# Optimization experiments

Hardware: AMD Instinct MI355X
Metric: run time of the kernel (lower is better)

The kernel has to match this reference:

```python
import jax, jax.numpy as jnp
import numpy as np

B, T, D, HD = 256, 256, 384, 64  # batch, seq_len, embedding_dim, head_dim


def setup_inputs() -> dict:
    key = jax.random.key(0)
    k1, k2, k3, k4 = jax.random.split(key, 4)
    x = jax.random.normal(k1, (B, T, D), dtype=jnp.float32)
    # nn.Linear(D, HD, bias=False) weight shape is [HD, D]; init scaled like kaiming-uniform magnitude
    Wq = jax.random.normal(k2, (HD, D), dtype=jnp.float32) * (1.0 / np.sqrt(D))
    Wk = jax.random.normal(k3, (HD, D), dtype=jnp.float32) * (1.0 / np.sqrt(D))
    Wv = jax.random.normal(k4, (HD, D), dtype=jnp.float32) * (1.0 / np.sqrt(D))
    return {"x": x, "Wq": Wq, "Wk": Wk, "Wv": Wv}


def reference(x, Wq, Wk, Wv):
    # Projections: x @ W^T  (Linear with bias=False)
    q = jnp.einsum('btd,hd->bth', x, Wq)  # [B,T,HD]
    k = jnp.einsum('btd,hd->bth', x, Wk)
    v = jnp.einsum('btd,hd->bth', x, Wv)
    scale = 1.0 / np.sqrt(HD).astype(np.float32)
    scores = jnp.einsum('bqh,bkh->bqk', q, k) * scale  # [B,T,T]
    T_ = x.shape[1]
    causal = jnp.tril(jnp.ones((T_, T_), dtype=bool))
    scores = jnp.where(causal, scores, jnp.float32(-jnp.inf))
    attn = jax.nn.softmax(scores, axis=-1)
    # dropout disabled (eval mode) for deterministic reference
    return jnp.einsum('bqk,bkh->bqh', attn, v)
```

## Files before the change

kernel.cpp:

```cpp
#include <hip/hip_runtime.h>

typedef __attribute__((ext_vector_type(8))) short bf16x8;
typedef __attribute__((ext_vector_type(4))) float f32x4;

__device__ inline unsigned short f2bf(float f) {
    unsigned u = __float_as_uint(f);
    return (unsigned short)((u + 0x7fffu + ((u >> 16) & 1u)) >> 16);
}
__device__ inline void gload16(const void* g, void* l) {
    __builtin_amdgcn_global_load_lds(
        (const __attribute__((address_space(1))) unsigned*)g,
        (__attribute__((address_space(3))) unsigned*)l, 16, 0, 0);
}

__global__ void wconv(const float* __restrict__ Wq, const float* __restrict__ Wk,
                      const float* __restrict__ Wv, short* __restrict__ Wp) {
    int i = blockIdx.x * 256 + threadIdx.x;
    if (i >= 192 * 384) return;
    int col = i / 384;
    int k   = i - col * 384;
    const float* src = col < 64 ? (Wq + col * 384)
                     : col < 128 ? (Wk + (col - 64) * 384)
                                 : (Wv + (col - 128) * 384);
    int kc = k >> 5, g = (k >> 3) & 3, kl = k & 7;
    Wp[kc * 6144 + (((g * 192 + col) ^ g) << 3) + kl] = (short)f2bf(src[k]);
}

__global__ __launch_bounds__(1024) void fused_attn(
    const float* __restrict__ x, const short* __restrict__ Wp,
    float* __restrict__ out) {
    __shared__ short LDSH[45568];
    short* const Ksh = LDSH;
    short* const Vt  = LDSH + 18432;
    short* const Pb  = LDSH + 35328;
    short* const wst = LDSH;
    short* const xst = LDSH + 18432;

    const int tid = threadIdx.x;
    const int wv = tid >> 6, lane = tid & 63;
    const int g = lane >> 4, c = lane & 15;
    const int b = blockIdx.x;
    const int q0 = wv * 16;

    const int xr0 = tid >> 3;
    const int xc4 = tid & 7;
    const float* gx0 = x + ((size_t)b * 256 + xr0) * 384 + xc4 * 4;
    const float* gx1 = gx0 + (size_t)128 * 384;

    f32x4 acc[12];
#pragma unroll
    for (int j = 0; j < 12; ++j) acc[j] = (f32x4){0.f, 0.f, 0.f, 0.f};

#define STAGE_W(S, BUF)                                                       \
    if (wv < 12) gload16(Wp + (S) * 6144 + wv * 512 + lane * 8,               \
                         wst + (BUF) * 6144 + wv * 512);
#define XWRITE(BUF, A, Bv)                                                    \
    {                                                                         \
        uint2 p0_, p1_;                                                       \
        p0_.x = (unsigned)f2bf((A).x) | ((unsigned)f2bf((A).y) << 16);        \
        p0_.y = (unsigned)f2bf((A).z) | ((unsigned)f2bf((A).w) << 16);        \
        p1_.x = (unsigned)f2bf((Bv).x) | ((unsigned)f2bf((Bv).y) << 16);      \
        p1_.y = (unsigned)f2bf((Bv).z) | ((unsigned)f2bf((Bv).w) << 16);      \
        *(uint2*)&xst[(BUF) * 10240 + xr0 * 40 + xc4 * 4] = p0_;              \
        *(uint2*)&xst[(BUF) * 10240 + (xr0 + 128) * 40 + xc4 * 4] = p1_;      \
    }
#define COMPUTE(S)                                                            \
    {                                                                         \
        const short* xb = xst + ((S) & 1) * 10240;                            \
        const short* wb = wst + ((S) & 1) * 6144;                             \
        bf16x8 af = *(const bf16x8*)&xb[(q0 + c) * 40 + g * 8];               \
        _Pragma("unroll")                                                     \
        for (int h_ = 0; h_ < 2; ++h_) {                                      \
            bf16x8 bfr[6];                                                    \
            _Pragma("unroll")                                                 \
            for (int j6 = 0; j6 < 6; ++j6) {                                  \
                int col = (h_ * 6 + j6) * 16 + c;                             \
                bfr[j6] = *(const bf16x8*)&wb[((g * 192 + col) ^ g) << 3];    \
            }                                                                 \
            _Pragma("unroll")                                                 \
            for (int j6 = 0; j6 < 6; ++j6)                                    \
                acc[h_ * 6 + j6] = __builtin_amdgcn_mfma_f32_16x16x32_bf16(   \
                    af, bfr[j6], acc[h_ * 6 + j6], 0, 0, 0);                  \
    }                                                                         \
    }
#define STEP(S, LX0, LX1, WX0, WX1)                                          \
    {                                                                        \
        STAGE_W((S) + 1, ((S) + 1) & 1)                                      \
        __builtin_amdgcn_sched_barrier(0);                                   \
        if ((S) <= 9) {                                                      \
            LX0 = *(const float4*)(gx0 + ((S) + 2) * 32);                    \
            LX1 = *(const float4*)(gx1 + ((S) + 2) * 32);                    \
        }                                                                    \
        __builtin_amdgcn_sched_barrier(0);                                   \
        COMPUTE(S)                                                           \
        XWRITE(((S) + 1) & 1, WX0, WX1)                                      \
        if (wv < 12) {                                                       \
            if ((S) <= 9) asm volatile("s_waitcnt vmcnt(2)" ::: "memory");   \
            else          asm volatile("s_waitcnt vmcnt(0)" ::: "memory");   \
        }                                                                    \
        asm volatile("s_waitcnt lgkmcnt(0)" ::: "memory");                   \
        __builtin_amdgcn_s_barrier();                                        \
        __builtin_amdgcn_sched_barrier(0);                                   \
    }

    float4 xA0, xA1, xB0, xB1, xC0, xC1;

    xA0 = *(const float4*)(gx0);
    xA1 = *(const float4*)(gx1);
    __builtin_amdgcn_sched_barrier(0);
    STAGE_W(0, 0)
    __builtin_amdgcn_sched_barrier(0);
    xB0 = *(const float4*)(gx0 + 32);
    xB1 = *(const float4*)(gx1 + 32);
    __builtin_amdgcn_sched_barrier(0);
    XWRITE(0, xA0, xA1)
    if (wv < 12) asm volatile("s_waitcnt vmcnt(2)" ::: "memory");
    asm volatile("s_waitcnt lgkmcnt(0)" ::: "memory");
    __builtin_amdgcn_s_barrier();
    __builtin_amdgcn_sched_barrier(0);

    STEP(0, xC0, xC1, xB0, xB1)
    STEP(1, xA0, xA1, xC0, xC1)
    STEP(2, xB0, xB1, xA0, xA1)
    STEP(3, xC0, xC1, xB0, xB1)
    STEP(4, xA0, xA1, xC0, xC1)
    STEP(5, xB0, xB1, xA0, xA1)
    STEP(6, xC0, xC1, xB0, xB1)
    STEP(7, xA0, xA1, xC0, xC1)
    STEP(8, xB0, xB1, xA0, xA1)
    STEP(9, xC0, xC1, xB0, xB1)
    STEP(10, xA0, xA1, xC0, xC1)
    COMPUTE(11)
    __syncthreads();

    short* const pbw = Pb + wv * 640;
    bf16x8 qf0, qf1;
    {
#pragma unroll
        for (int r = 0; r < 4; ++r) {
            pbw[(4 * g + r) * 40 + c]      = (short)f2bf(acc[0][r]);
            pbw[(4 * g + r) * 40 + 16 + c] = (short)f2bf(acc[1][r]);
        }
        qf0 = *(const bf16x8*)&pbw[c * 40 + g * 8];
#pragma unroll
        for (int r = 0; r < 4; ++r) {
            pbw[(4 * g + r) * 40 + c]      = (short)f2bf(acc[2][r]);
            pbw[(4 * g + r) * 40 + 16 + c] = (short)f2bf(acc[3][r]);
        }
        qf1 = *(const bf16x8*)&pbw[c * 40 + g * 8];
    }
#pragma unroll
    for (int nj = 4; nj < 8; ++nj) {
        const int row = q0 + 4 * g;
#pragma unroll
        for (int r = 0; r < 4; ++r)
            Ksh[(row + r) * 72 + (nj - 4) * 16 + c] = (short)f2bf(acc[nj][r]);
    }
#pragma unroll
    for (int nj = 8; nj < 12; ++nj) {
        const int h = (nj - 8) * 16 + c;
        const int swz = ((h >> 3) & 7) << 3;
        const int row = q0 + 4 * g;
#pragma unroll
        for (int r = 0; r < 4; ++r)
            Vt[(h * 264 + row + r) ^ swz] = (short)f2bf(acc[nj][r]);
    }
    __syncthreads();

    {
        f32x4 o[4];
#pragma unroll
        for (int nj = 0; nj < 4; ++nj) o[nj] = (f32x4){0.f, 0.f, 0.f, 0.f};
        float m[4] = {-INFINITY, -INFINITY, -INFINITY, -INFINITY};
        float ls[4] = {0.f, 0.f, 0.f, 0.f};
        const int jmax = (q0 + 15) >> 5;

        for (int j = 0; j <= jmax; ++j) {
            f32x4 s0 = {0.f, 0.f, 0.f, 0.f}, s1 = {0.f, 0.f, 0.f, 0.f};
            {
                bf16x8 kf;
                kf = *(const bf16x8*)&Ksh[(32 * j + c) * 72 + g * 8];
                s0 = __builtin_amdgcn_mfma_f32_16x16x32_bf16(qf0, kf, s0, 0, 0, 0);
                kf = *(const bf16x8*)&Ksh[(32 * j + c) * 72 + 32 + g * 8];
                s0 = __builtin_amdgcn_mfma_f32_16x16x32_bf16(qf1, kf, s0, 0, 0, 0);
                kf = *(const bf16x8*)&Ksh[(32 * j + 16 + c) * 72 + g * 8];
                s1 = __builtin_amdgcn_mfma_f32_16x16x32_bf16(qf0, kf, s1, 0, 0, 0);
                kf = *(const bf16x8*)&Ksh[(32 * j + 16 + c) * 72 + 32 + g * 8];
                s1 = __builtin_amdgcn_mfma_f32_16x16x32_bf16(qf1, kf, s1, 0, 0, 0);
            }
            float t0[4], t1[4];
#pragma unroll
            for (int r = 0; r < 4; ++r) {
                t0[r] = s0[r] * 0.125f;
                t1[r] = s1[r] * 0.125f;
            }
            if (j == jmax) {
                int q = q0 + 4 * g;
#pragma unroll
                for (int r = 0; r < 4; ++r) {
                    if (32 * j + c > q + r) t0[r] = -INFINITY;
                    if (32 * j + 16 + c > q + r) t1[r] = -INFINITY;
                }
            }
            float corr[4], p0[4], p1[4];
#pragma unroll
            for (int r = 0; r < 4; ++r) {
                float v = fmaxf(t0[r], t1[r]);
#pragma unroll
                for (int off = 1; off < 16; off <<= 1) v = fmaxf(v, __shfl_xor(v, off, 16));
                float mn = fmaxf(m[r], v);
                corr[r] = __expf(m[r] - mn);
                m[r] = mn;
                p0[r] = __expf(t0[r] - mn);
                p1[r] = __expf(t1[r] - mn);
                float rs = p0[r] + p1[r];
#pragma unroll
                for (int off = 1; off < 16; off <<= 1) rs += __shfl_xor(rs, off, 16);
                ls[r] = ls[r] * corr[r] + rs;
            }
#pragma unroll
            for (int nj = 0; nj < 4; ++nj) {
                f32x4 t = o[nj];
                t[0] *= corr[0]; t[1] *= corr[1]; t[2] *= corr[2]; t[3] *= corr[3];
                o[nj] = t;
            }
#pragma unroll
            for (int r = 0; r < 4; ++r) {
                pbw[(4 * g + r) * 40 + c]      = (short)f2bf(p0[r]);
                pbw[(4 * g + r) * 40 + 16 + c] = (short)f2bf(p1[r]);
            }
            bf16x8 pfa = *(const bf16x8*)&pbw[c * 40 + g * 8];
#pragma unroll
            for (int nj = 0; nj < 4; ++nj) {
                int h = 16 * nj + c;
                int swz = ((2 * nj + (c >> 3)) & 7) << 3;
                bf16x8 vf = *(const bf16x8*)&Vt[(h * 264 + 32 * j + g * 8) ^ swz];
                o[nj] = __builtin_amdgcn_mfma_f32_16x16x32_bf16(pfa, vf, o[nj], 0, 0, 0);
            }
        }
        float inv[4];
#pragma unroll
        for (int r = 0; r < 4; ++r) inv[r] = 1.f / ls[r];
        float* ob = out + ((size_t)b * 256 + q0) * 64;
#pragma unroll
        for (int nj = 0; nj < 4; ++nj)
#pragma unroll
            for (int r = 0; r < 4; ++r)
                ob[(4 * g + r) * 64 + 16 * nj + c] = o[nj][r] * inv[r];
    }
#undef STAGE_W
#undef XWRITE
#undef COMPUTE
#undef STEP
}

extern "C" void kernel_launch(void* const* d_in, const int* in_sizes, int n_in,
                              void* d_out, int out_size, void* d_ws, size_t ws_size,
                              hipStream_t stream) {
    const float* x  = (const float*)d_in[0];
    const float* Wq = (const float*)d_in[1];
    const float* Wk = (const float*)d_in[2];
    const float* Wv = (const float*)d_in[3];
    float* out = (float*)d_out;

    short* Wp = (short*)d_ws;

    wconv<<<dim3(288), dim3(256), 0, stream>>>(Wq, Wk, Wv, Wp);
    fused_attn<<<dim3(256), dim3(1024), 0, stream>>>(x, Wp, out);
}
```

Measured before the change: 41.10 us.

## Retile projection GEMM to 64x48 per-wave blocks and stage Q through LDS

The QKV projection GEMM tiling changes from each wave owning 16 rows by all 192 columns to a 4x4 wave grid in which each wave owns a 64x48 output tile. Per K step each wave now reads 4 A fragments and 3 B fragments for 12 MFMAs instead of 1 A and 12 B, which cuts LDS read traffic. Because a wave no longer holds its own Q rows, Q is written to a new LDS region and read back before attention. This raises shared memory use from about 89KB to 125KB and adds a Q store-and-reload round trip.

```diff
diff --git a/kernel.cpp b/kernel.cpp
--- a/kernel.cpp
+++ b/kernel.cpp
@@ -29,27 +29,32 @@
 __global__ __launch_bounds__(1024) void fused_attn(
     const float* __restrict__ x, const short* __restrict__ Wp,
     float* __restrict__ out) {
-    __shared__ short LDSH[45568];
-    short* const Ksh = LDSH;
-    short* const Vt  = LDSH + 18432;
-    short* const Pb  = LDSH + 35328;
-    short* const wst = LDSH;
-    short* const xst = LDSH + 18432;
+    __shared__ short LDSH[64000];
+    short* const Qlds = LDSH;
+    short* const Ksh  = LDSH + 18432;
+    short* const Vt   = LDSH + 36864;
+    short* const Pb   = LDSH + 53760;
+    short* const wst  = LDSH;
+    short* const xst  = LDSH + 18432;
 
     const int tid = threadIdx.x;
     const int wv = tid >> 6, lane = tid & 63;
     const int g = lane >> 4, c = lane & 15;
     const int b = blockIdx.x;
     const int q0 = wv * 16;
+    const int wm2 = (wv >> 2) * 64;
+    const int wn2 = (wv & 3) * 48;
 
     const int xr0 = tid >> 3;
     const int xc4 = tid & 7;
     const float* gx0 = x + ((size_t)b * 256 + xr0) * 384 + xc4 * 4;
     const float* gx1 = gx0 + (size_t)128 * 384;
 
-    f32x4 acc[12];
-#pragma unroll
-    for (int j = 0; j < 12; ++j) acc[j] = (f32x4){0.f, 0.f, 0.f, 0.f};
+    f32x4 acc[4][3];
+#pragma unroll
+    for (int i = 0; i < 4; ++i)
+#pragma unroll
+        for (int j = 0; j < 3; ++j) acc[i][j] = (f32x4){0.f, 0.f, 0.f, 0.f};
 
 #define STAGE_W(S, BUF)                                                       \
     if (wv < 12) gload16(Wp + (S) * 6144 + wv * 512 + lane * 8,               \
@@ -68,28 +73,29 @@
     {                                                                         \
         const short* xb = xst + ((S) & 1) * 10240;                            \
         const short* wb = wst + ((S) & 1) * 6144;                             \
-        bf16x8 af = *(const bf16x8*)&xb[(q0 + c) * 40 + g * 8];               \
+        bf16x8 af[4], bfr[3];                                                 \
         _Pragma("unroll")                                                     \
-        for (int h_ = 0; h_ < 2; ++h_) {                                      \
-            bf16x8 bfr[6];                                                    \
+        for (int mi = 0; mi < 4; ++mi)                                        \
+            af[mi] = *(const bf16x8*)&xb[(wm2 + 16 * mi + c) * 40 + g * 8];   \
+        _Pragma("unroll")                                                     \
+        for (int nj = 0; nj < 3; ++nj) {                                      \
+            int col = wn2 + nj * 16 + c;                                      \
+            bfr[nj] = *(const bf16x8*)&wb[((g * 192 + col) ^ g) << 3];        \
+        }                                                                     \
+        _Pragma("unroll")                                                     \
+        for (int mi = 0; mi < 4; ++mi)                                        \
             _Pragma("unroll")                                                 \
-            for (int j6 = 0; j6 < 6; ++j6) {                                  \
-                int col = (h_ * 6 + j6) * 16 + c;                             \
-                bfr[j6] = *(const bf16x8*)&wb[((g * 192 + col) ^ g) << 3];    \
-            }                                                                 \
-            _Pragma("unroll")                                                 \
-            for (int j6 = 0; j6 < 6; ++j6)                                    \
-                acc[h_ * 6 + j6] = __builtin_amdgcn_mfma_f32_16x16x32_bf16(   \
-                    af, bfr[j6], acc[h_ * 6 + j6], 0, 0, 0);                  \
-    }                                                                         \
-    }
-#define STEP(S, LX0, LX1, WX0, WX1)                                          \
+            for (int nj = 0; nj < 3; ++nj)                                    \
+                acc[mi][nj] = __builtin_amdgcn_mfma_f32_16x16x32_bf16(        \
+                    af[mi], bfr[nj], acc[mi][nj], 0, 0, 0);                   \
+    }
+#define STEP(S, LD0, LD1, WX0, WX1)                                          \
     {                                                                        \
         STAGE_W((S) + 1, ((S) + 1) & 1)                                      \
         __builtin_amdgcn_sched_barrier(0);                                   \
         if ((S) <= 9) {                                                      \
-            LX0 = *(const float4*)(gx0 + ((S) + 2) * 32);                    \
-            LX1 = *(const float4*)(gx1 + ((S) + 2) * 32);                    \
+            LD0 = *(const float4*)(gx0 + ((S) + 2) * 32);                    \
+            LD1 = *(const float4*)(gx1 + ((S) + 2) * 32);                    \
         }                                                                    \
         __builtin_amdgcn_sched_barrier(0);                                   \
         COMPUTE(S)                                                           \
@@ -133,41 +139,35 @@
     COMPUTE(11)
     __syncthreads();
 
-    short* const pbw = Pb + wv * 640;
-    bf16x8 qf0, qf1;
+#pragma unroll
+    for (int mi = 0; mi < 4; ++mi) {
+#pragma unroll
+        for (int nj = 0; nj < 3; ++nj) {
+            const int colb = wn2 + nj * 16;
+            const int row = wm2 + 16 * mi + 4 * g;
+            if (colb < 64) {
+#pragma unroll
+                for (int r = 0; r < 4; ++r)
+                    Qlds[(row + r) * 72 + colb + c] = (short)f2bf(acc[mi][nj][r]);
+            } else if (colb < 128) {
+#pragma unroll
+                for (int r = 0; r < 4; ++r)
+                    Ksh[(row + r) * 72 + (colb - 64) + c] = (short)f2bf(acc[mi][nj][r]);
+            } else {
+                const int h = colb - 128 + c;
+                const int swz = ((h >> 3) & 7) << 3;
+#pragma unroll
+                for (int r = 0; r < 4; ++r)
+                    Vt[(h * 264 + row + r) ^ swz] = (short)f2bf(acc[mi][nj][r]);
+            }
+        }
+    }
+    __syncthreads();
+
     {
-#pragma unroll
-        for (int r = 0; r < 4; ++r) {
-            pbw[(4 * g + r) * 40 + c]      = (short)f2bf(acc[0][r]);
-            pbw[(4 * g + r) * 40 + 16 + c] = (short)f2bf(acc[1][r]);
-        }
-        qf0 = *(const bf16x8*)&pbw[c * 40 + g * 8];
-#pragma unroll
-        for (int r = 0; r < 4; ++r) {
-            pbw[(4 * g + r) * 40 + c]      = (short)f2bf(acc[2][r]);
-            pbw[(4 * g + r) * 40 + 16 + c] = (short)f2bf(acc[3][r]);
-        }
-        qf1 = *(const bf16x8*)&pbw[c * 40 + g * 8];
-    }
-#pragma unroll
-    for (int nj = 4; nj < 8; ++nj) {
-        const int row = q0 + 4 * g;
-#pragma unroll
-        for (int r = 0; r < 4; ++r)
-            Ksh[(row + r) * 72 + (nj - 4) * 16 + c] = (short)f2bf(acc[nj][r]);
-    }
-#pragma unroll
-    for (int nj = 8; nj < 12; ++nj) {
-        const int h = (nj - 8) * 16 + c;
-        const int swz = ((h >> 3) & 7) << 3;
-        const int row = q0 + 4 * g;
-#pragma unroll
-        for (int r = 0; r < 4; ++r)
-            Vt[(h * 264 + row + r) ^ swz] = (short)f2bf(acc[nj][r]);
-    }
-    __syncthreads();
-
-    {
+        short* const pbw = Pb + wv * 640;
+        bf16x8 qf0 = *(const bf16x8*)&Qlds[(q0 + c) * 72 + g * 8];
+        bf16x8 qf1 = *(const bf16x8*)&Qlds[(q0 + c) * 72 + 32 + g * 8];
         f32x4 o[4];
 #pragma unroll
         for (int nj = 0; nj < 4; ++nj) o[nj] = (f32x4){0.f, 0.f, 0.f, 0.f};
```

Result: no change. 41.72 us (+1.5%).

## Process two K-chunks per barrier in QKV projection pipeline with 4-slot LDS ring

Applied to the files above, without the earlier changes.

Restructures the projection pipeline to stage and compute two 32-wide K chunks per step, using a four-slot LDS ring for x and W tiles instead of double buffering. This halves the number of block-wide barriers and waitcnt stalls across the 12 chunks and deepens prefetch. In exchange it enlarges LDS to 128 KB per block and holds more float4 registers in flight. The vmcnt wait is now applied to all waves, not only those issuing W loads.

```diff
diff --git a/kernel.cpp b/kernel.cpp
--- a/kernel.cpp
+++ b/kernel.cpp
@@ -29,12 +29,12 @@
 __global__ __launch_bounds__(1024) void fused_attn(
     const float* __restrict__ x, const short* __restrict__ Wp,
     float* __restrict__ out) {
-    __shared__ short LDSH[45568];
+    __shared__ short LDSH[65536];
+    short* const xst = LDSH;
+    short* const wst = LDSH + 40960;
     short* const Ksh = LDSH;
     short* const Vt  = LDSH + 18432;
     short* const Pb  = LDSH + 35328;
-    short* const wst = LDSH;
-    short* const xst = LDSH + 18432;
 
     const int tid = threadIdx.x;
     const int wv = tid >> 6, lane = tid & 63;
@@ -51,9 +51,10 @@
 #pragma unroll
     for (int j = 0; j < 12; ++j) acc[j] = (f32x4){0.f, 0.f, 0.f, 0.f};
 
-#define STAGE_W(S, BUF)                                                       \
-    if (wv < 12) gload16(Wp + (S) * 6144 + wv * 512 + lane * 8,               \
-                         wst + (BUF) * 6144 + wv * 512);
+#define STAGE_W1(K)                                                           \
+    if (wv < 12) gload16(Wp + (K) * 6144 + wv * 512 + lane * 8,               \
+                         wst + ((K) & 3) * 6144 + wv * 512);
+#define STAGE_W2(K)  STAGE_W1(K) STAGE_W1((K) + 1)
 #define XWRITE(BUF, A, Bv)                                                    \
     {                                                                         \
         uint2 p0_, p1_;                                                       \
@@ -61,13 +62,20 @@
         p0_.y = (unsigned)f2bf((A).z) | ((unsigned)f2bf((A).w) << 16);        \
         p1_.x = (unsigned)f2bf((Bv).x) | ((unsigned)f2bf((Bv).y) << 16);      \
         p1_.y = (unsigned)f2bf((Bv).z) | ((unsigned)f2bf((Bv).w) << 16);      \
-        *(uint2*)&xst[(BUF) * 10240 + xr0 * 40 + xc4 * 4] = p0_;              \
-        *(uint2*)&xst[(BUF) * 10240 + (xr0 + 128) * 40 + xc4 * 4] = p1_;      \
-    }
-#define COMPUTE(S)                                                            \
+        *(uint2*)&xst[((BUF) & 3) * 10240 + xr0 * 40 + xc4 * 4] = p0_;        \
+        *(uint2*)&xst[((BUF) & 3) * 10240 + (xr0 + 128) * 40 + xc4 * 4] = p1_;\
+    }
+#define LOADSET(P0, P1, P2, P3, K)                                            \
+    P0 = *(const float4*)(gx0 + (K) * 32);                                    \
+    P1 = *(const float4*)(gx1 + (K) * 32);                                    \
+    P2 = *(const float4*)(gx0 + ((K) + 1) * 32);                              \
+    P3 = *(const float4*)(gx1 + ((K) + 1) * 32);
+#define WRITESET(P0, P1, P2, P3, K)                                           \
+    XWRITE((K), P0, P1) XWRITE((K) + 1, P2, P3)
+#define COMPUTE1(K)                                                           \
     {                                                                         \
-        const short* xb = xst + ((S) & 1) * 10240;                            \
-        const short* wb = wst + ((S) & 1) * 6144;                             \
+        const short* xb = xst + ((K) & 3) * 10240;                            \
+        const short* wb = wst + ((K) & 3) * 6144;                             \
         bf16x8 af = *(const bf16x8*)&xb[(q0 + c) * 40 + g * 8];               \
         _Pragma("unroll")                                                     \
         for (int h_ = 0; h_ < 2; ++h_) {                                      \
@@ -81,56 +89,60 @@
             for (int j6 = 0; j6 < 6; ++j6)                                    \
                 acc[h_ * 6 + j6] = __builtin_amdgcn_mfma_f32_16x16x32_bf16(   \
                     af, bfr[j6], acc[h_ * 6 + j6], 0, 0, 0);                  \
-    }                                                                         \
-    }
-#define STEP(S, LX0, LX1, WX0, WX1)                                          \
-    {                                                                        \
-        STAGE_W((S) + 1, ((S) + 1) & 1)                                      \
-        __builtin_amdgcn_sched_barrier(0);                                   \
-        if ((S) <= 9) {                                                      \
-            LX0 = *(const float4*)(gx0 + ((S) + 2) * 32);                    \
-            LX1 = *(const float4*)(gx1 + ((S) + 2) * 32);                    \
-        }                                                                    \
-        __builtin_amdgcn_sched_barrier(0);                                   \
-        COMPUTE(S)                                                           \
-        XWRITE(((S) + 1) & 1, WX0, WX1)                                      \
-        if (wv < 12) {                                                       \
-            if ((S) <= 9) asm volatile("s_waitcnt vmcnt(2)" ::: "memory");   \
-            else          asm volatile("s_waitcnt vmcnt(0)" ::: "memory");   \
-        }                                                                    \
-        asm volatile("s_waitcnt lgkmcnt(0)" ::: "memory");                   \
-        __builtin_amdgcn_s_barrier();                                        \
-        __builtin_amdgcn_sched_barrier(0);                                   \
-    }
-
-    float4 xA0, xA1, xB0, xB1, xC0, xC1;
-
-    xA0 = *(const float4*)(gx0);
-    xA1 = *(const float4*)(gx1);
-    __builtin_amdgcn_sched_barrier(0);
-    STAGE_W(0, 0)
-    __builtin_amdgcn_sched_barrier(0);
-    xB0 = *(const float4*)(gx0 + 32);
-    xB1 = *(const float4*)(gx1 + 32);
-    __builtin_amdgcn_sched_barrier(0);
-    XWRITE(0, xA0, xA1)
-    if (wv < 12) asm volatile("s_waitcnt vmcnt(2)" ::: "memory");
-    asm volatile("s_waitcnt lgkmcnt(0)" ::: "memory");
-    __builtin_amdgcn_s_barrier();
-    __builtin_amdgcn_sched_barrier(0);
-
-    STEP(0, xC0, xC1, xB0, xB1)
-    STEP(1, xA0, xA1, xC0, xC1)
-    STEP(2, xB0, xB1, xA0, xA1)
-    STEP(3, xC0, xC1, xB0, xB1)
-    STEP(4, xA0, xA1, xC0, xC1)
-    STEP(5, xB0, xB1, xA0, xA1)
-    STEP(6, xC0, xC1, xB0, xB1)
-    STEP(7, xA0, xA1, xC0, xC1)
-    STEP(8, xB0, xB1, xA0, xA1)
-    STEP(9, xC0, xC1, xB0, xB1)
-    STEP(10, xA0, xA1, xC0, xC1)
-    COMPUTE(11)
+        }                                                                     \
+    }
+#define COMPUTE2(K)  COMPUTE1(K) COMPUTE1((K) + 1)
+#define ENDSTEP(N)                                                            \
+    asm volatile("s_waitcnt vmcnt(" #N ")" ::: "memory");                     \
+    asm volatile("s_waitcnt lgkmcnt(0)" ::: "memory");                        \
+    __builtin_amdgcn_s_barrier();                                             \
+    __builtin_amdgcn_sched_barrier(0);
+
+    float4 xA0, xA1, xA2, xA3, xB0, xB1, xB2, xB3, xC0, xC1, xC2, xC3;
+
+    LOADSET(xA0, xA1, xA2, xA3, 0)
+    __builtin_amdgcn_sched_barrier(0);
+    STAGE_W2(0)
+    __builtin_amdgcn_sched_barrier(0);
+    LOADSET(xB0, xB1, xB2, xB3, 2)
+    __builtin_amdgcn_sched_barrier(0);
+    WRITESET(xA0, xA1, xA2, xA3, 0)
+    ENDSTEP(4)
+
+    STAGE_W2(2)
+    __builtin_amdgcn_sched_barrier(0);
+    LOADSET(xC0, xC1, xC2, xC3, 4)
+    __builtin_amdgcn_sched_barrier(0);
+    COMPUTE2(0)
+    WRITESET(xB0, xB1, xB2, xB3, 2)
+    ENDSTEP(4)
+    STAGE_W2(4)
+    __builtin_amdgcn_sched_barrier(0);
+    LOADSET(xA0, xA1, xA2, xA3, 6)
+    __builtin_amdgcn_sched_barrier(0);
+    COMPUTE2(2)
+    WRITESET(xC0, xC1, xC2, xC3, 4)
+    ENDSTEP(4)
+    STAGE_W2(6)
+    __builtin_amdgcn_sched_barrier(0);
+    LOADSET(xB0, xB1, xB2, xB3, 8)
+    __builtin_amdgcn_sched_barrier(0);
+    COMPUTE2(4)
+    WRITESET(xA0, xA1, xA2, xA3, 6)
+    ENDSTEP(4)
+    STAGE_W2(8)
+    __builtin_amdgcn_sched_barrier(0);
+    LOADSET(xC0, xC1, xC2, xC3, 10)
+    __builtin_amdgcn_sched_barrier(0);
+    COMPUTE2(6)
+    WRITESET(xB0, xB1, xB2, xB3, 8)
+    ENDSTEP(4)
+    STAGE_W2(10)
+    __builtin_amdgcn_sched_barrier(0);
+    COMPUTE2(8)
+    WRITESET(xC0, xC1, xC2, xC3, 10)
+    ENDSTEP(0)
+    COMPUTE2(10)
     __syncthreads();
 
     short* const pbw = Pb + wv * 640;
@@ -248,10 +260,14 @@
             for (int r = 0; r < 4; ++r)
                 ob[(4 * g + r) * 64 + 16 * nj + c] = o[nj][r] * inv[r];
     }
-#undef STAGE_W
+#undef STAGE_W1
+#undef STAGE_W2
 #undef XWRITE
-#undef COMPUTE
-#undef STEP
+#undef LOADSET
+#undef WRITESET
+#undef COMPUTE1
+#undef COMPUTE2
+#undef ENDSTEP
 }
 
 extern "C" void kernel_launch(void* const* d_in, const int* in_sizes, int n_in,
```

Result: slower. 49.00 us (+19.2%).
